# Performance work log

Measured on AMD Instinct MI355X. Metric: run time of the kernel, lower is better.

Reference implementation:

```python
import jax, jax.numpy as jnp
import numpy as np


def setup_inputs() -> dict:
    key = jax.random.key(0)
    ks = jax.random.split(key, 4)
    B, C, H, W = 8, 512, 128, 128
    K, D = 150, 512
    std = 0.02
    return {
        "x": jax.random.normal(ks[0], (B, C, H, W), dtype=jnp.float32),
        "cls_repr": jax.random.normal(ks[1], (1, K, D), dtype=jnp.float32) * std,
        "W_cls": jax.random.normal(ks[2], (D, D), dtype=jnp.float32) * std,
        "W_feat": jax.random.normal(ks[3], (D, D), dtype=jnp.float32) * std,
        "ln_gamma": jnp.ones((K,), dtype=jnp.float32),
        "ln_beta": jnp.zeros((K,), dtype=jnp.float32),
    }


def reference(x, cls_repr, W_cls, W_feat, ln_gamma, ln_beta):
    b, c, h, w = x.shape
    K = cls_repr.shape[1]
    # img_feat: [b, hw, c]
    img_feat = jnp.transpose(x, (0, 2, 3, 1)).reshape(b, h * w, c)
    cls = jnp.broadcast_to(cls_repr, (b, K, c))
    # coupled_attn: [b, K, hw]
    coupled_attn = jnp.einsum("bnc,bkc->bkn", img_feat, cls)
    # class-direction softmax over hw, feeds class offsets
    cls_attn = jax.nn.softmax(coupled_attn, axis=2)                 # [b,K,hw]
    cls_offset = jnp.einsum("bkn,bnc->bkc", cls_attn, img_feat) @ W_cls.T
    aligned_cls = cls + cls_offset                                   # [b,K,c]
    # position-direction softmax over K, feeds feature offsets
    pos_attn = jax.nn.softmax(coupled_attn, axis=1)                 # [b,K,hw]
    feat_offset = jnp.einsum("bkn,bkc->bnc", pos_attn, cls) @ W_feat.T
    aligned_feat = img_feat + feat_offset                            # [b,hw,c]
    # masks: [b, hw, K], LayerNorm over K
    masks = jnp.einsum("bnc,bkc->bnk", aligned_feat, aligned_cls)
    mu = jnp.mean(masks, axis=-1, keepdims=True)
    var = jnp.var(masks, axis=-1, keepdims=True)
    masks = (masks - mu) * jax.lax.rsqrt(var + 1e-5) * ln_gamma + ln_beta
    return jnp.transpose(masks, (0, 2, 1)).reshape(b, K, h, w)
```

## Files before the change

kernel.cpp:

```cpp
#include <hip/hip_runtime.h>
#include <math.h>

#define BB 8
#define CC 512
#define HWN 16384
#define KK 150
#define KP 160
#define NSEG 16
#define SEGN (HWN / NSEG)

typedef short bf8v __attribute__((ext_vector_type(8)));
typedef float f4v __attribute__((ext_vector_type(4)));

static __device__ inline unsigned short f2b(float f) {
  unsigned u = __float_as_uint(f);
  u += 0x7fffu + ((u >> 16) & 1u);
  return (unsigned short)(u >> 16);
}
static __device__ inline float b2f(unsigned short s) {
  return __uint_as_float(((unsigned)s) << 16);
}
static __device__ inline float b2fs(short s) { return b2f((unsigned short)s); }

__global__ __launch_bounds__(256) void t0_prep(const float* __restrict__ cls,
                                               const float* __restrict__ Wc,
                                               const float* __restrict__ Wf,
                                               unsigned short* __restrict__ cls16,
                                               unsigned short* __restrict__ Wc16,
                                               unsigned short* __restrict__ Wf16,
                                               unsigned short* __restrict__ MT16,
                                               unsigned short* __restrict__ AC16) {
  int i = blockIdx.x * 256 + threadIdx.x;
  if (i < KP * CC) {
    int k = i >> 9, c = i & 511;
    cls16[i] = (k < KK) ? f2b(cls[k * CC + c]) : 0;
  }
  if (i < BB * KP * KP) MT16[i] = 0;
  if (i < BB * (KP - KK) * CC) {
    int b = i / ((KP - KK) * CC);
    int r = i % ((KP - KK) * CC);
    int k = KK + (r >> 9);
    int c = r & 511;
    AC16[((size_t)b * KP + k) * CC + c] = 0;
  }
  if (i < CC * CC) {
    Wc16[i] = f2b(Wc[i]);
    Wf16[i] = f2b(Wf[i]);
  }
}

__global__ __launch_bounds__(256) void t1_transpose(const float* __restrict__ x,
                                                    unsigned short* __restrict__ xT,
                                                    unsigned short* __restrict__ x16) {
  __shared__ float ts[32][65];
  const int n0 = blockIdx.x * 64, c0 = blockIdx.y * 32, b = blockIdx.z;
  const int tid = threadIdx.x;
  const float* xb = x + (size_t)b * CC * HWN;
  unsigned short* x16o = x16 + (size_t)b * CC * HWN;
#pragma unroll
  for (int i = 0; i < 8; i++) {
    int e = tid + i * 256;
    int n = e & 63, c = e >> 6;
    float v = xb[(size_t)(c0 + c) * HWN + n0 + n];
    ts[c][n] = v;
    x16o[(size_t)(c0 + c) * HWN + n0 + n] = f2b(v);
  }
  __syncthreads();
  unsigned short* xo = xT + (size_t)b * HWN * CC;
#pragma unroll
  for (int i = 0; i < 4; i++) {
    int e = tid + i * 256;
    int c2 = e & 15, n = e >> 4;
    unsigned vv = (unsigned)f2b(ts[2 * c2][n]) | ((unsigned)f2b(ts[2 * c2 + 1][n]) << 16);
    *(unsigned*)&xo[(size_t)(n0 + n) * CC + c0 + 2 * c2] = vv;
  }
}

__global__ __launch_bounds__(256) void g1_mfma(const unsigned short* __restrict__ xT,
                                               const unsigned short* __restrict__ cls16,
                                               unsigned short* __restrict__ E16,
                                               unsigned short* __restrict__ ET16,
                                               float* __restrict__ vvec) {
  const int n0 = blockIdx.x * 128, b = blockIdx.y;
  const int tid = threadIdx.x, w = tid >> 6, L = tid & 63;
  const int q = L >> 4, m16 = L & 15;
  f4v zf = {0.f, 0.f, 0.f, 0.f};
  f4v acc[10][2];
#pragma unroll
  for (int mt = 0; mt < 10; mt++) { acc[mt][0] = zf; acc[mt][1] = zf; }
  const unsigned short* xr0 = xT + ((size_t)(b * HWN + n0 + 32 * w + m16)) * CC + 8 * q;
  const unsigned short* xr1 = xr0 + 16 * CC;
  const unsigned short* cb = cls16 + (size_t)m16 * CC + 8 * q;
#pragma unroll 2
  for (int c0 = 0; c0 < CC; c0 += 32) {
    bf8v b0 = *(const bf8v*)(xr0 + c0);
    bf8v b1 = *(const bf8v*)(xr1 + c0);
#pragma unroll
    for (int mt = 0; mt < 10; mt++) {
      bf8v a = *(const bf8v*)(cb + (size_t)(16 * mt) * CC + c0);
      acc[mt][0] = __builtin_amdgcn_mfma_f32_16x16x32_bf16(a, b0, acc[mt][0], 0, 0, 0);
      acc[mt][1] = __builtin_amdgcn_mfma_f32_16x16x32_bf16(a, b1, acc[mt][1], 0, 0, 0);
    }
  }
  float cs0 = 0.f, cs1 = 0.f;
#pragma unroll
  for (int mt = 0; mt < 10; mt++)
#pragma unroll
    for (int r = 0; r < 4; r++) {
      int k = 16 * mt + 4 * q + r;
      bool valid = k < KK;
      float e0 = valid ? __expf(acc[mt][0][r]) : 0.f;
      float e1 = valid ? __expf(acc[mt][1][r]) : 0.f;
      acc[mt][0][r] = e0;
      acc[mt][1][r] = e1;
      cs0 += e0;
      cs1 += e1;
    }
#pragma unroll
  for (int mt = 0; mt < 10; mt++)
#pragma unroll
    for (int r = 0; r < 4; r++) {
      int k = 16 * mt + 4 * q + r;
      size_t row = ((size_t)(b * KP + k)) * HWN + n0 + 32 * w;
      E16[row + m16] = f2b(acc[mt][0][r]);
      E16[row + 16 + m16] = f2b(acc[mt][1][r]);
    }
  const int nA = n0 + 32 * w + m16;
#pragma unroll
  for (int mt = 0; mt < 10; mt++) {
    unsigned lo0 = (unsigned)f2b(acc[mt][0][0]) | ((unsigned)f2b(acc[mt][0][1]) << 16);
    unsigned hi0 = (unsigned)f2b(acc[mt][0][2]) | ((unsigned)f2b(acc[mt][0][3]) << 16);
    unsigned lo1 = (unsigned)f2b(acc[mt][1][0]) | ((unsigned)f2b(acc[mt][1][1]) << 16);
    unsigned hi1 = (unsigned)f2b(acc[mt][1][2]) | ((unsigned)f2b(acc[mt][1][3]) << 16);
    size_t eoff = ((size_t)(b * HWN + nA)) * KP + 16 * mt + 4 * q;
    *(uint2*)&ET16[eoff] = make_uint2(lo0, hi0);
    *(uint2*)&ET16[eoff + (size_t)16 * KP] = make_uint2(lo1, hi1);
  }
  cs0 += __shfl_xor(cs0, 16, 64);
  cs0 += __shfl_xor(cs0, 32, 64);
  cs1 += __shfl_xor(cs1, 16, 64);
  cs1 += __shfl_xor(cs1, 32, 64);
  if (q == 0) {
    vvec[b * HWN + nA] = 1.0f / cs0;
    vvec[b * HWN + nA + 16] = 1.0f / cs1;
  }
}

__global__ __launch_bounds__(256) void g2_rowsum(const unsigned short* __restrict__ E16,
                                                 float* __restrict__ rowsum) {
  const int bk = blockIdx.x;
  const int b = bk / KK, k = bk % KK;
  const bf8v* row = (const bf8v*)(E16 + ((size_t)(b * KP + k)) * HWN);
  __shared__ float red[4];
  const int tid = threadIdx.x, lane = tid & 63, w = tid >> 6;
  float s = 0.f;
  for (int i = tid; i < HWN / 8; i += 256) {
    bf8v u = row[i];
#pragma unroll
    for (int j = 0; j < 8; j++) s += b2fs(u[j]);
  }
#pragma unroll
  for (int o = 32; o > 0; o >>= 1) s += __shfl_down(s, o, 64);
  if (lane == 0) red[w] = s;
  __syncthreads();
  if (tid == 0) rowsum[bk] = red[0] + red[1] + red[2] + red[3];
}

__global__ __launch_bounds__(256) void g3_mfma(const unsigned short* __restrict__ x16,
                                               const unsigned short* __restrict__ E16,
                                               float* __restrict__ Scp) {
  const int cblk = blockIdx.x, seg = blockIdx.y, b = blockIdx.z;
  const int tid = threadIdx.x, w = tid >> 6, L = tid & 63;
  const int q = L >> 4, m16 = L & 15;
  f4v zf = {0.f, 0.f, 0.f, 0.f};
  f4v acc[10][2];
#pragma unroll
  for (int mt = 0; mt < 10; mt++) { acc[mt][0] = zf; acc[mt][1] = zf; }
  const unsigned short* eb = E16 + ((size_t)(b * KP + m16)) * HWN + 8 * q;
  const unsigned short* xb = x16 + ((size_t)(b * CC + cblk * 128 + 32 * w + m16)) * HWN + 8 * q;
  const int ns0 = seg * SEGN;
#pragma unroll 2
  for (int nc0 = ns0; nc0 < ns0 + SEGN; nc0 += 32) {
    bf8v x0 = *(const bf8v*)(xb + nc0);
    bf8v x1 = *(const bf8v*)(xb + (size_t)16 * HWN + nc0);
#pragma unroll
    for (int mt = 0; mt < 10; mt++) {
      bf8v a = *(const bf8v*)(eb + (size_t)(16 * mt) * HWN + nc0);
      acc[mt][0] = __builtin_amdgcn_mfma_f32_16x16x32_bf16(a, x0, acc[mt][0], 0, 0, 0);
      acc[mt][1] = __builtin_amdgcn_mfma_f32_16x16x32_bf16(a, x1, acc[mt][1], 0, 0, 0);
    }
  }
#pragma unroll
  for (int mt = 0; mt < 10; mt++)
#pragma unroll
    for (int cc = 0; cc < 2; cc++)
#pragma unroll
      for (int r = 0; r < 4; r++) {
        int k = 16 * mt + 4 * q + r;
        if (k < KK) {
          int c = cblk * 128 + 32 * w + 16 * cc + m16;
          Scp[(((size_t)(b * NSEG + seg)) * KK + k) * CC + c] = acc[mt][cc][r];
        }
      }
}

__global__ __launch_bounds__(256) void g5_reduce(const float* __restrict__ Scp,
                                                 const float* __restrict__ rowsum,
                                                 unsigned short* __restrict__ Sc16) {
  const int bk = blockIdx.x;
  const int b = bk / KK, k = bk % KK;
  const float inv = 1.0f / rowsum[bk];
  for (int c = threadIdx.x; c < CC; c += 256) {
    float s = 0.f;
    for (int g = 0; g < NSEG; g++)
      s += Scp[(((size_t)(b * NSEG + g)) * KK + k) * CC + c];
    Sc16[((size_t)b * KP + k) * CC + c] = f2b(s * inv);
  }
}

__global__ __launch_bounds__(256) void g4b_cwf(const unsigned short* __restrict__ cls16,
                                               const unsigned short* __restrict__ Wf16,
                                               unsigned short* __restrict__ CWf16) {
  const int tid = threadIdx.x, w = tid >> 6, L = tid & 63;
  const int q = L >> 4, m16 = L & 15;
  const int j0 = blockIdx.x * 128 + 32 * w;
  f4v zf = {0.f, 0.f, 0.f, 0.f};
  f4v acc[10][2];
#pragma unroll
  for (int mt = 0; mt < 10; mt++) { acc[mt][0] = zf; acc[mt][1] = zf; }
  const unsigned short* ar = cls16 + (size_t)m16 * CC + 8 * q;
  const unsigned short* br = Wf16 + (size_t)(j0 + m16) * CC + 8 * q;
#pragma unroll 2
  for (int c0 = 0; c0 < CC; c0 += 32) {
    bf8v b0 = *(const bf8v*)(br + c0);
    bf8v b1 = *(const bf8v*)(br + (size_t)16 * CC + c0);
#pragma unroll
    for (int mt = 0; mt < 10; mt++) {
      bf8v a = *(const bf8v*)(ar + (size_t)(16 * mt) * CC + c0);
      acc[mt][0] = __builtin_amdgcn_mfma_f32_16x16x32_bf16(a, b0, acc[mt][0], 0, 0, 0);
      acc[mt][1] = __builtin_amdgcn_mfma_f32_16x16x32_bf16(a, b1, acc[mt][1], 0, 0, 0);
    }
  }
#pragma unroll
  for (int mt = 0; mt < 10; mt++)
#pragma unroll
    for (int nc = 0; nc < 2; nc++)
#pragma unroll
      for (int r = 0; r < 4; r++) {
        int k1 = 16 * mt + 4 * q + r;
        int j = j0 + 16 * nc + m16;
        CWf16[(size_t)k1 * CC + j] = f2b(acc[mt][nc][r]);
      }
}

__global__ __launch_bounds__(256) void g4a_ac(const unsigned short* __restrict__ Sc16,
                                              const unsigned short* __restrict__ Wc16,
                                              const float* __restrict__ cls,
                                              unsigned short* __restrict__ AC16) {
  const int b = blockIdx.y;
  const int tid = threadIdx.x, w = tid >> 6, L = tid & 63;
  const int q = L >> 4, m16 = L & 15;
  const int j0 = blockIdx.x * 128 + 32 * w;
  f4v zf = {0.f, 0.f, 0.f, 0.f};
  f4v acc[10][2];
#pragma unroll
  for (int mt = 0; mt < 10; mt++) { acc[mt][0] = zf; acc[mt][1] = zf; }
  const unsigned short* ar = Sc16 + ((size_t)b * KP + m16) * CC + 8 * q;
  const unsigned short* br = Wc16 + (size_t)(j0 + m16) * CC + 8 * q;
#pragma unroll 2
  for (int c0 = 0; c0 < CC; c0 += 32) {
    bf8v b0 = *(const bf8v*)(br + c0);
    bf8v b1 = *(const bf8v*)(br + (size_t)16 * CC + c0);
#pragma unroll
    for (int mt = 0; mt < 10; mt++) {
      bf8v a = *(const bf8v*)(ar + (size_t)(16 * mt) * CC + c0);
      acc[mt][0] = __builtin_amdgcn_mfma_f32_16x16x32_bf16(a, b0, acc[mt][0], 0, 0, 0);
      acc[mt][1] = __builtin_amdgcn_mfma_f32_16x16x32_bf16(a, b1, acc[mt][1], 0, 0, 0);
    }
  }
#pragma unroll
  for (int mt = 0; mt < 10; mt++)
#pragma unroll
    for (int nc = 0; nc < 2; nc++)
#pragma unroll
      for (int r = 0; r < 4; r++) {
        int k = 16 * mt + 4 * q + r;
        if (k < KK) {
          int j = j0 + 16 * nc + m16;
          AC16[((size_t)b * KP + k) * CC + j] = f2b(cls[k * CC + j] + acc[mt][nc][r]);
        }
      }
}

__global__ __launch_bounds__(256) void g4c_m(const unsigned short* __restrict__ AC16,
                                             const unsigned short* __restrict__ CWf16,
                                             unsigned short* __restrict__ MT16) {
  const int b = blockIdx.y;
  const int tid = threadIdx.x, w = tid >> 6, L = tid & 63;
  const int q = L >> 4, m16 = L & 15;
  const int k1t = blockIdx.x * 64 + 16 * w;
  f4v zf = {0.f, 0.f, 0.f, 0.f};
  f4v acc[10];
#pragma unroll
  for (int mt = 0; mt < 10; mt++) acc[mt] = zf;
  const unsigned short* ar = AC16 + ((size_t)b * KP + m16) * CC + 8 * q;
  const unsigned short* br = CWf16 + (size_t)(k1t + m16) * CC + 8 * q;
#pragma unroll 2
  for (int c0 = 0; c0 < CC; c0 += 32) {
    bf8v bb = *(const bf8v*)(br + c0);
#pragma unroll
    for (int mt = 0; mt < 10; mt++) {
      bf8v a = *(const bf8v*)(ar + (size_t)(16 * mt) * CC + c0);
      acc[mt] = __builtin_amdgcn_mfma_f32_16x16x32_bf16(a, bb, acc[mt], 0, 0, 0);
    }
  }
  const int k1 = k1t + m16;
#pragma unroll
  for (int mt = 0; mt < 10; mt++)
#pragma unroll
    for (int r = 0; r < 4; r++) {
      int k2 = 16 * mt + 4 * q + r;
      if (k1 < KK) MT16[((size_t)b * KP + k2) * KP + k1] = f2b(acc[mt][r]);
    }
}

__global__ __launch_bounds__(256) void g6_mfma(
    const unsigned short* __restrict__ xT, const unsigned short* __restrict__ ET,
    const float* __restrict__ vvec, const unsigned short* __restrict__ AC16,
    const unsigned short* __restrict__ MT16, const float* __restrict__ gamma,
    const float* __restrict__ beta, float* __restrict__ out) {
  const int n0 = blockIdx.x * 128, b = blockIdx.y;
  const int tid = threadIdx.x, w = tid >> 6, L = tid & 63;
  const int q = L >> 4, m16 = L & 15;
  f4v zf = {0.f, 0.f, 0.f, 0.f};
  f4v acc[10][2];
#pragma unroll
  for (int mt = 0; mt < 10; mt++) { acc[mt][0] = zf; acc[mt][1] = zf; }

  const unsigned short* et0 = ET + ((size_t)(b * HWN + n0 + 32 * w + m16)) * KP + 8 * q;
  const unsigned short* et1 = et0 + 16 * KP;
  const unsigned short* mb = MT16 + (size_t)b * KP * KP + (size_t)m16 * KP + 8 * q;
#pragma unroll
  for (int kc = 0; kc < KP; kc += 32) {
    bf8v b0 = *(const bf8v*)(et0 + kc);
    bf8v b1 = *(const bf8v*)(et1 + kc);
#pragma unroll
    for (int mt = 0; mt < 10; mt++) {
      bf8v a = *(const bf8v*)(mb + (size_t)(16 * mt) * KP + kc);
      acc[mt][0] = __builtin_amdgcn_mfma_f32_16x16x32_bf16(a, b0, acc[mt][0], 0, 0, 0);
      acc[mt][1] = __builtin_amdgcn_mfma_f32_16x16x32_bf16(a, b1, acc[mt][1], 0, 0, 0);
    }
  }
  const float v0 = vvec[b * HWN + n0 + 32 * w + m16];
  const float v1 = vvec[b * HWN + n0 + 32 * w + 16 + m16];
#pragma unroll
  for (int mt = 0; mt < 10; mt++)
#pragma unroll
    for (int r = 0; r < 4; r++) {
      acc[mt][0][r] *= v0;
      acc[mt][1][r] *= v1;
    }

  const unsigned short* xr0 = xT + ((size_t)(b * HWN + n0 + 32 * w + m16)) * CC + 8 * q;
  const unsigned short* xr1 = xr0 + 16 * CC;
  const unsigned short* ab = AC16 + (size_t)b * KP * CC + (size_t)m16 * CC + 8 * q;
#pragma unroll 2
  for (int c0 = 0; c0 < CC; c0 += 32) {
    bf8v b0 = *(const bf8v*)(xr0 + c0);
    bf8v b1 = *(const bf8v*)(xr1 + c0);
#pragma unroll
    for (int mt = 0; mt < 10; mt++) {
      bf8v a = *(const bf8v*)(ab + (size_t)(16 * mt) * CC + c0);
      acc[mt][0] = __builtin_amdgcn_mfma_f32_16x16x32_bf16(a, b0, acc[mt][0], 0, 0, 0);
      acc[mt][1] = __builtin_amdgcn_mfma_f32_16x16x32_bf16(a, b1, acc[mt][1], 0, 0, 0);
    }
  }

  float s1[2] = {0.f, 0.f}, s2[2] = {0.f, 0.f};
#pragma unroll
  for (int mt = 0; mt < 10; mt++)
#pragma unroll
    for (int r = 0; r < 4; r++)
#pragma unroll
      for (int nc = 0; nc < 2; nc++) {
        float a = acc[mt][nc][r];
        s1[nc] += a;
        s2[nc] += a * a;
      }
#pragma unroll
  for (int nc = 0; nc < 2; nc++) {
    s1[nc] += __shfl_xor(s1[nc], 16, 64);
    s1[nc] += __shfl_xor(s1[nc], 32, 64);
    s2[nc] += __shfl_xor(s2[nc], 16, 64);
    s2[nc] += __shfl_xor(s2[nc], 32, 64);
  }
  float mu[2], inv[2];
#pragma unroll
  for (int nc = 0; nc < 2; nc++) {
    mu[nc] = s1[nc] * (1.0f / KK);
    float var = s2[nc] * (1.0f / KK) - mu[nc] * mu[nc];
    inv[nc] = rsqrtf(var + 1e-5f);
  }
#pragma unroll
  for (int mt = 0; mt < 10; mt++)
#pragma unroll
    for (int r = 0; r < 4; r++) {
      int k = 16 * mt + 4 * q + r;
      if (k < KK) {
        float g = gamma[k], be = beta[k];
        size_t row = (size_t)(b * KK + k) * HWN + n0 + 32 * w;
        out[row + m16] = (acc[mt][0][r] - mu[0]) * inv[0] * g + be;
        out[row + 16 + m16] = (acc[mt][1][r] - mu[1]) * inv[1] * g + be;
      }
    }
}

extern "C" void kernel_launch(void* const* d_in, const int* in_sizes, int n_in,
                              void* d_out, int out_size, void* d_ws, size_t ws_size,
                              hipStream_t stream) {
  const float* x = (const float*)d_in[0];
  const float* cls = (const float*)d_in[1];
  const float* Wc = (const float*)d_in[2];
  const float* Wf = (const float*)d_in[3];
  const float* gam = (const float*)d_in[4];
  const float* bet = (const float*)d_in[5];
  float* out = (float*)d_out;

  char* p = (char*)d_ws;
  auto alloc = [&](size_t bytes) {
    char* r = p;
    p += (bytes + 255) & ~(size_t)255;
    return r;
  };
  unsigned short* xT16 = (unsigned short*)alloc((size_t)BB * HWN * CC * 2);
  unsigned short* x16 = (unsigned short*)alloc((size_t)BB * CC * HWN * 2);
  unsigned short* E16 = (unsigned short*)alloc((size_t)BB * KP * HWN * 2);
  unsigned short* ET16 = (unsigned short*)alloc((size_t)BB * HWN * KP * 2);
  float* Scp = (float*)alloc((size_t)BB * NSEG * KK * CC * 4);
  unsigned short* Sc16 = (unsigned short*)alloc((size_t)BB * KP * CC * 2);
  unsigned short* AC16 = (unsigned short*)alloc((size_t)BB * KP * CC * 2);
  unsigned short* CWf16 = (unsigned short*)alloc((size_t)192 * CC * 2);
  unsigned short* cls16 = (unsigned short*)alloc((size_t)KP * CC * 2);
  unsigned short* Wc16 = (unsigned short*)alloc((size_t)CC * CC * 2);
  unsigned short* Wf16 = (unsigned short*)alloc((size_t)CC * CC * 2);
  unsigned short* MT16 = (unsigned short*)alloc((size_t)BB * KP * KP * 2);
  float* rowsum = (float*)alloc(BB * KK * 4);
  float* vvec = (float*)alloc((size_t)BB * HWN * 4);

  t0_prep<<<dim3((CC * CC + 255) / 256), 256, 0, stream>>>(cls, Wc, Wf, cls16, Wc16,
                                                           Wf16, MT16, AC16);
  t1_transpose<<<dim3(HWN / 64, CC / 32, BB), 256, 0, stream>>>(x, xT16, x16);
  g1_mfma<<<dim3(HWN / 128, BB), 256, 0, stream>>>(xT16, cls16, E16, ET16, vvec);
  g2_rowsum<<<dim3(BB * KK), 256, 0, stream>>>(E16, rowsum);
  g4b_cwf<<<dim3(CC / 128), 256, 0, stream>>>(cls16, Wf16, CWf16);
  g3_mfma<<<dim3(CC / 128, NSEG, BB), 256, 0, stream>>>(x16, E16, Scp);
  g5_reduce<<<dim3(BB * KK), 256, 0, stream>>>(Scp, rowsum, Sc16);
  g4a_ac<<<dim3(CC / 128, BB), 256, 0, stream>>>(Sc16, Wc16, cls, AC16);
  g4c_m<<<dim3(3, BB), 256, 0, stream>>>(AC16, CWf16, MT16);
  g6_mfma<<<dim3(HWN / 128, BB), 256, 0, stream>>>(xT16, ET16, vvec, AC16, MT16,
                                                   gam, bet, out);
}
```

Measured before the change: 867.9 us.

## Widen MFMA n-tiles to 64 per wave and vectorize transpose loads

The g1 and g6 MFMA kernels now give each wave 64 spatial columns (four 16-wide tiles) instead of 32. Each A-fragment load from the class or matrix operand is therefore reused across four MFMAs, which cuts global/L2 traffic for that operand, and the grid halves. The transpose kernel switches to float4 loads and ushort4 stores to raise memory efficiency. The cost is doubled accumulator register use (160 floats), which lowers occupancy and could cause spills, and fewer blocks per batch.

```diff
diff --git a/kernel.cpp b/kernel.cpp
--- a/kernel.cpp
+++ b/kernel.cpp
@@ -58,21 +58,33 @@
   const float* xb = x + (size_t)b * CC * HWN;
   unsigned short* x16o = x16 + (size_t)b * CC * HWN;
 #pragma unroll
-  for (int i = 0; i < 8; i++) {
+  for (int i = 0; i < 2; i++) {
     int e = tid + i * 256;
-    int n = e & 63, c = e >> 6;
-    float v = xb[(size_t)(c0 + c) * HWN + n0 + n];
-    ts[c][n] = v;
-    x16o[(size_t)(c0 + c) * HWN + n0 + n] = f2b(v);
+    int c = e >> 4, n4 = (e & 15) * 4;
+    float4 v = *(const float4*)&xb[(size_t)(c0 + c) * HWN + n0 + n4];
+    ts[c][n4] = v.x;
+    ts[c][n4 + 1] = v.y;
+    ts[c][n4 + 2] = v.z;
+    ts[c][n4 + 3] = v.w;
+    ushort4 pk;
+    pk.x = f2b(v.x);
+    pk.y = f2b(v.y);
+    pk.z = f2b(v.z);
+    pk.w = f2b(v.w);
+    *(ushort4*)&x16o[(size_t)(c0 + c) * HWN + n0 + n4] = pk;
   }
   __syncthreads();
   unsigned short* xo = xT + (size_t)b * HWN * CC;
 #pragma unroll
-  for (int i = 0; i < 4; i++) {
+  for (int i = 0; i < 2; i++) {
     int e = tid + i * 256;
-    int c2 = e & 15, n = e >> 4;
-    unsigned vv = (unsigned)f2b(ts[2 * c2][n]) | ((unsigned)f2b(ts[2 * c2 + 1][n]) << 16);
-    *(unsigned*)&xo[(size_t)(n0 + n) * CC + c0 + 2 * c2] = vv;
+    int cg = e & 7, n = e >> 3;
+    ushort4 pk;
+    pk.x = f2b(ts[4 * cg][n]);
+    pk.y = f2b(ts[4 * cg + 1][n]);
+    pk.z = f2b(ts[4 * cg + 2][n]);
+    pk.w = f2b(ts[4 * cg + 3][n]);
+    *(ushort4*)&xo[(size_t)(n0 + n) * CC + c0 + 4 * cg] = pk;
   }
 }
 
@@ -81,68 +93,74 @@
                                                unsigned short* __restrict__ E16,
                                                unsigned short* __restrict__ ET16,
                                                float* __restrict__ vvec) {
-  const int n0 = blockIdx.x * 128, b = blockIdx.y;
-  const int tid = threadIdx.x, w = tid >> 6, L = tid & 63;
-  const int q = L >> 4, m16 = L & 15;
-  f4v zf = {0.f, 0.f, 0.f, 0.f};
-  f4v acc[10][2];
-#pragma unroll
-  for (int mt = 0; mt < 10; mt++) { acc[mt][0] = zf; acc[mt][1] = zf; }
-  const unsigned short* xr0 = xT + ((size_t)(b * HWN + n0 + 32 * w + m16)) * CC + 8 * q;
-  const unsigned short* xr1 = xr0 + 16 * CC;
+  const int n0 = blockIdx.x * 256, b = blockIdx.y;
+  const int tid = threadIdx.x, w = tid >> 6, L = tid & 63;
+  const int q = L >> 4, m16 = L & 15;
+  f4v zf = {0.f, 0.f, 0.f, 0.f};
+  f4v acc[10][4];
+#pragma unroll
+  for (int mt = 0; mt < 10; mt++)
+#pragma unroll
+    for (int nc = 0; nc < 4; nc++) acc[mt][nc] = zf;
+  const unsigned short* xr = xT + ((size_t)(b * HWN + n0 + 64 * w + m16)) * CC + 8 * q;
   const unsigned short* cb = cls16 + (size_t)m16 * CC + 8 * q;
 #pragma unroll 2
   for (int c0 = 0; c0 < CC; c0 += 32) {
-    bf8v b0 = *(const bf8v*)(xr0 + c0);
-    bf8v b1 = *(const bf8v*)(xr1 + c0);
+    bf8v bv[4];
+#pragma unroll
+    for (int nc = 0; nc < 4; nc++)
+      bv[nc] = *(const bf8v*)(xr + (size_t)(16 * nc) * CC + c0);
 #pragma unroll
     for (int mt = 0; mt < 10; mt++) {
       bf8v a = *(const bf8v*)(cb + (size_t)(16 * mt) * CC + c0);
-      acc[mt][0] = __builtin_amdgcn_mfma_f32_16x16x32_bf16(a, b0, acc[mt][0], 0, 0, 0);
-      acc[mt][1] = __builtin_amdgcn_mfma_f32_16x16x32_bf16(a, b1, acc[mt][1], 0, 0, 0);
-    }
-  }
-  float cs0 = 0.f, cs1 = 0.f;
+#pragma unroll
+      for (int nc = 0; nc < 4; nc++)
+        acc[mt][nc] = __builtin_amdgcn_mfma_f32_16x16x32_bf16(a, bv[nc], acc[mt][nc], 0, 0, 0);
+    }
+  }
+  float cs[4] = {0.f, 0.f, 0.f, 0.f};
 #pragma unroll
   for (int mt = 0; mt < 10; mt++)
 #pragma unroll
     for (int r = 0; r < 4; r++) {
       int k = 16 * mt + 4 * q + r;
       bool valid = k < KK;
-      float e0 = valid ? __expf(acc[mt][0][r]) : 0.f;
-      float e1 = valid ? __expf(acc[mt][1][r]) : 0.f;
-      acc[mt][0][r] = e0;
-      acc[mt][1][r] = e1;
-      cs0 += e0;
-      cs1 += e1;
+#pragma unroll
+      for (int nc = 0; nc < 4; nc++) {
+        float e = valid ? __expf(acc[mt][nc][r]) : 0.f;
+        acc[mt][nc][r] = e;
+        cs[nc] += e;
+      }
     }
 #pragma unroll
   for (int mt = 0; mt < 10; mt++)
 #pragma unroll
     for (int r = 0; r < 4; r++) {
       int k = 16 * mt + 4 * q + r;
-      size_t row = ((size_t)(b * KP + k)) * HWN + n0 + 32 * w;
-      E16[row + m16] = f2b(acc[mt][0][r]);
-      E16[row + 16 + m16] = f2b(acc[mt][1][r]);
-    }
-  const int nA = n0 + 32 * w + m16;
-#pragma unroll
-  for (int mt = 0; mt < 10; mt++) {
-    unsigned lo0 = (unsigned)f2b(acc[mt][0][0]) | ((unsigned)f2b(acc[mt][0][1]) << 16);
-    unsigned hi0 = (unsigned)f2b(acc[mt][0][2]) | ((unsigned)f2b(acc[mt][0][3]) << 16);
-    unsigned lo1 = (unsigned)f2b(acc[mt][1][0]) | ((unsigned)f2b(acc[mt][1][1]) << 16);
-    unsigned hi1 = (unsigned)f2b(acc[mt][1][2]) | ((unsigned)f2b(acc[mt][1][3]) << 16);
-    size_t eoff = ((size_t)(b * HWN + nA)) * KP + 16 * mt + 4 * q;
-    *(uint2*)&ET16[eoff] = make_uint2(lo0, hi0);
-    *(uint2*)&ET16[eoff + (size_t)16 * KP] = make_uint2(lo1, hi1);
-  }
-  cs0 += __shfl_xor(cs0, 16, 64);
-  cs0 += __shfl_xor(cs0, 32, 64);
-  cs1 += __shfl_xor(cs1, 16, 64);
-  cs1 += __shfl_xor(cs1, 32, 64);
+      size_t row = ((size_t)(b * KP + k)) * HWN + n0 + 64 * w;
+#pragma unroll
+      for (int nc = 0; nc < 4; nc++)
+        E16[row + 16 * nc + m16] = f2b(acc[mt][nc][r]);
+    }
+  const int nA = n0 + 64 * w + m16;
+#pragma unroll
+  for (int mt = 0; mt < 10; mt++)
+#pragma unroll
+    for (int nc = 0; nc < 4; nc++) {
+      unsigned lo = (unsigned)f2b(acc[mt][nc][0]) | ((unsigned)f2b(acc[mt][nc][1]) << 16);
+      unsigned hi = (unsigned)f2b(acc[mt][nc][2]) | ((unsigned)f2b(acc[mt][nc][3]) << 16);
+      size_t eoff = ((size_t)(b * HWN + nA + 16 * nc)) * KP + 16 * mt + 4 * q;
+      *(uint2*)&ET16[eoff] = make_uint2(lo, hi);
+    }
+#pragma unroll
+  for (int nc = 0; nc < 4; nc++) {
+    cs[nc] += __shfl_xor(cs[nc], 16, 64);
+    cs[nc] += __shfl_xor(cs[nc], 32, 64);
+  }
   if (q == 0) {
-    vvec[b * HWN + nA] = 1.0f / cs0;
-    vvec[b * HWN + nA + 16] = 1.0f / cs1;
+#pragma unroll
+    for (int nc = 0; nc < 4; nc++)
+      vvec[b * HWN + nA + 16 * nc] = 1.0f / cs[nc];
   }
 }
 
@@ -329,74 +347,80 @@
     const float* __restrict__ vvec, const unsigned short* __restrict__ AC16,
     const unsigned short* __restrict__ MT16, const float* __restrict__ gamma,
     const float* __restrict__ beta, float* __restrict__ out) {
-  const int n0 = blockIdx.x * 128, b = blockIdx.y;
-  const int tid = threadIdx.x, w = tid >> 6, L = tid & 63;
-  const int q = L >> 4, m16 = L & 15;
-  f4v zf = {0.f, 0.f, 0.f, 0.f};
-  f4v acc[10][2];
-#pragma unroll
-  for (int mt = 0; mt < 10; mt++) { acc[mt][0] = zf; acc[mt][1] = zf; }
-
-  const unsigned short* et0 = ET + ((size_t)(b * HWN + n0 + 32 * w + m16)) * KP + 8 * q;
-  const unsigned short* et1 = et0 + 16 * KP;
+  const int n0 = blockIdx.x * 256, b = blockIdx.y;
+  const int tid = threadIdx.x, w = tid >> 6, L = tid & 63;
+  const int q = L >> 4, m16 = L & 15;
+  f4v zf = {0.f, 0.f, 0.f, 0.f};
+  f4v acc[10][4];
+#pragma unroll
+  for (int mt = 0; mt < 10; mt++)
+#pragma unroll
+    for (int nc = 0; nc < 4; nc++) acc[mt][nc] = zf;
+
+  const unsigned short* et = ET + ((size_t)(b * HWN + n0 + 64 * w + m16)) * KP + 8 * q;
   const unsigned short* mb = MT16 + (size_t)b * KP * KP + (size_t)m16 * KP + 8 * q;
 #pragma unroll
   for (int kc = 0; kc < KP; kc += 32) {
-    bf8v b0 = *(const bf8v*)(et0 + kc);
-    bf8v b1 = *(const bf8v*)(et1 + kc);
+    bf8v bv[4];
+#pragma unroll
+    for (int nc = 0; nc < 4; nc++)
+      bv[nc] = *(const bf8v*)(et + (size_t)(16 * nc) * KP + kc);
 #pragma unroll
     for (int mt = 0; mt < 10; mt++) {
       bf8v a = *(const bf8v*)(mb + (size_t)(16 * mt) * KP + kc);
-      acc[mt][0] = __builtin_amdgcn_mfma_f32_16x16x32_bf16(a, b0, acc[mt][0], 0, 0, 0);
-      acc[mt][1] = __builtin_amdgcn_mfma_f32_16x16x32_bf16(a, b1, acc[mt][1], 0, 0, 0);
-    }
-  }
-  const float v0 = vvec[b * HWN + n0 + 32 * w + m16];
-  const float v1 = vvec[b * HWN + n0 + 32 * w + 16 + m16];
-#pragma unroll
-  for (int mt = 0; mt < 10; mt++)
-#pragma unroll
-    for (int r = 0; r < 4; r++) {
-      acc[mt][0][r] *= v0;
-      acc[mt][1][r] *= v1;
-    }
-
-  const unsigned short* xr0 = xT + ((size_t)(b * HWN + n0 + 32 * w + m16)) * CC + 8 * q;
-  const unsigned short* xr1 = xr0 + 16 * CC;
+#pragma unroll
+      for (int nc = 0; nc < 4; nc++)
+        acc[mt][nc] = __builtin_amdgcn_mfma_f32_16x16x32_bf16(a, bv[nc], acc[mt][nc], 0, 0, 0);
+    }
+  }
+  float vs[4];
+#pragma unroll
+  for (int nc = 0; nc < 4; nc++) vs[nc] = vvec[b * HWN + n0 + 64 * w + 16 * nc + m16];
+#pragma unroll
+  for (int mt = 0; mt < 10; mt++)
+#pragma unroll
+    for (int nc = 0; nc < 4; nc++)
+#pragma unroll
+      for (int r = 0; r < 4; r++) acc[mt][nc][r] *= vs[nc];
+
+  const unsigned short* xr = xT + ((size_t)(b * HWN + n0 + 64 * w + m16)) * CC + 8 * q;
   const unsigned short* ab = AC16 + (size_t)b * KP * CC + (size_t)m16 * CC + 8 * q;
 #pragma unroll 2
   for (int c0 = 0; c0 < CC; c0 += 32) {
-    bf8v b0 = *(const bf8v*)(xr0 + c0);
-    bf8v b1 = *(const bf8v*)(xr1 + c0);
+    bf8v bv[4];
+#pragma unroll
+    for (int nc = 0; nc < 4; nc++)
+      bv[nc] = *(const bf8v*)(xr + (size_t)(16 * nc) * CC + c0);
 #pragma unroll
     for (int mt = 0; mt < 10; mt++) {
       bf8v a = *(const bf8v*)(ab + (size_t)(16 * mt) * CC + c0);
-      acc[mt][0] = __builtin_amdgcn_mfma_f32_16x16x32_bf16(a, b0, acc[mt][0], 0, 0, 0);
-      acc[mt][1] = __builtin_amdgcn_mfma_f32_16x16x32_bf16(a, b1, acc[mt][1], 0, 0, 0);
-    }
-  }
-
-  float s1[2] = {0.f, 0.f}, s2[2] = {0.f, 0.f};
+#pragma unroll
+      for (int nc = 0; nc < 4; nc++)
+        acc[mt][nc] = __builtin_amdgcn_mfma_f32_16x16x32_bf16(a, bv[nc], acc[mt][nc], 0, 0, 0);
+    }
+  }
+
+  float s1[4] = {0.f, 0.f, 0.f, 0.f}, s2[4] = {0.f, 0.f, 0.f, 0.f};
 #pragma unroll
   for (int mt = 0; mt < 10; mt++)
 #pragma unroll
     for (int r = 0; r < 4; r++)
 #pragma unroll
-      for (int nc = 0; nc < 2; nc++) {
+      for (int nc = 0; nc < 4; nc++) {
         float a = acc[mt][nc][r];
         s1[nc] += a;
         s2[nc] += a * a;
       }
 #pragma unroll
-  for (int nc = 0; nc < 2; nc++) {
+  for (int nc = 0; nc < 4; nc++) {
     s1[nc] += __shfl_xor(s1[nc], 16, 64);
     s1[nc] += __shfl_xor(s1[nc], 32, 64);
     s2[nc] += __shfl_xor(s2[nc], 16, 64);
     s2[nc] += __shfl_xor(s2[nc], 32, 64);
   }
-  float mu[2], inv[2];
-#pragma unroll
-  for (int nc = 0; nc < 2; nc++) {
+  float mu[4], inv[4];
+#pragma unroll
+  for (int nc = 0; nc < 4; nc++) {
     mu[nc] = s1[nc] * (1.0f / KK);
     float var = s2[nc] * (1.0f / KK) - mu[nc] * mu[nc];
     inv[nc] = rsqrtf(var + 1e-5f);
@@ -408,9 +432,10 @@
       int k = 16 * mt + 4 * q + r;
       if (k < KK) {
         float g = gamma[k], be = beta[k];
-        size_t row = (size_t)(b * KK + k) * HWN + n0 + 32 * w;
-        out[row + m16] = (acc[mt][0][r] - mu[0]) * inv[0] * g + be;
-        out[row + 16 + m16] = (acc[mt][1][r] - mu[1]) * inv[1] * g + be;
+        size_t row = (size_t)(b * KK + k) * HWN + n0 + 64 * w;
+#pragma unroll
+        for (int nc = 0; nc < 4; nc++)
+          out[row + 16 * nc + m16] = (acc[mt][nc][r] - mu[nc]) * inv[nc] * g + be;
       }
     }
 }
@@ -450,13 +475,13 @@
   t0_prep<<<dim3((CC * CC + 255) / 256), 256, 0, stream>>>(cls, Wc, Wf, cls16, Wc16,
                                                            Wf16, MT16, AC16);
   t1_transpose<<<dim3(HWN / 64, CC / 32, BB), 256, 0, stream>>>(x, xT16, x16);
-  g1_mfma<<<dim3(HWN / 128, BB), 256, 0, stream>>>(xT16, cls16, E16, ET16, vvec);
+  g1_mfma<<<dim3(HWN / 256, BB), 256, 0, stream>>>(xT16, cls16, E16, ET16, vvec);
   g2_rowsum<<<dim3(BB * KK), 256, 0, stream>>>(E16, rowsum);
   g4b_cwf<<<dim3(CC / 128), 256, 0, stream>>>(cls16, Wf16, CWf16);
   g3_mfma<<<dim3(CC / 128, NSEG, BB), 256, 0, stream>>>(x16, E16, Scp);
   g5_reduce<<<dim3(BB * KK), 256, 0, stream>>>(Scp, rowsum, Sc16);
   g4a_ac<<<dim3(CC / 128, BB), 256, 0, stream>>>(Sc16, Wc16, cls, AC16);
   g4c_m<<<dim3(3, BB), 256, 0, stream>>>(AC16, CWf16, MT16);
-  g6_mfma<<<dim3(HWN / 128, BB), 256, 0, stream>>>(xT16, ET16, vvec, AC16, MT16,
+  g6_mfma<<<dim3(HWN / 256, BB), 256, 0, stream>>>(xT16, ET16, vvec, AC16, MT16,
                                                    gam, bet, out);
 }
```

Result: no change. 853.0 us (-1.7%).

## Double-buffer xT tiles into LDS via direct global-to-LDS loads; vectorize transpose

Applied to the files above, without the earlier changes.

The two xT-consuming GEMM kernels (g1 and g6) now stage 128x32 bf16 tiles of xT into a double-buffered, XOR-swizzled LDS buffer using global_load_lds. The load for the next step is issued while MFMAs run on the current one, and in g6 the first stage is prefetched during the earlier ET×MT GEMM. The transpose kernel switches to float4 reads and ushort4 writes to cut the number of memory instructions. The cost is extra LDS use and a block barrier on every K-step, which may reduce occupancy.

```diff
diff --git a/kernel.cpp b/kernel.cpp
--- a/kernel.cpp
+++ b/kernel.cpp
@@ -21,6 +21,12 @@
   return __uint_as_float(((unsigned)s) << 16);
 }
 static __device__ inline float b2fs(short s) { return b2f((unsigned short)s); }
+
+typedef const __attribute__((address_space(1))) void* gas_p;
+typedef __attribute__((address_space(3))) void* las_p;
+static __device__ __forceinline__ void gload16(const void* gp, void* lp) {
+  __builtin_amdgcn_global_load_lds((gas_p)gp, (las_p)lp, 16, 0, 0);
+}
 
 __global__ __launch_bounds__(256) void t0_prep(const float* __restrict__ cls,
                                                const float* __restrict__ Wc,
@@ -58,21 +64,33 @@
   const float* xb = x + (size_t)b * CC * HWN;
   unsigned short* x16o = x16 + (size_t)b * CC * HWN;
 #pragma unroll
-  for (int i = 0; i < 8; i++) {
+  for (int i = 0; i < 2; i++) {
     int e = tid + i * 256;
-    int n = e & 63, c = e >> 6;
-    float v = xb[(size_t)(c0 + c) * HWN + n0 + n];
-    ts[c][n] = v;
-    x16o[(size_t)(c0 + c) * HWN + n0 + n] = f2b(v);
+    int c = e >> 4, n4 = (e & 15) * 4;
+    float4 v = *(const float4*)&xb[(size_t)(c0 + c) * HWN + n0 + n4];
+    ts[c][n4] = v.x;
+    ts[c][n4 + 1] = v.y;
+    ts[c][n4 + 2] = v.z;
+    ts[c][n4 + 3] = v.w;
+    ushort4 pk;
+    pk.x = f2b(v.x);
+    pk.y = f2b(v.y);
+    pk.z = f2b(v.z);
+    pk.w = f2b(v.w);
+    *(ushort4*)&x16o[(size_t)(c0 + c) * HWN + n0 + n4] = pk;
   }
   __syncthreads();
   unsigned short* xo = xT + (size_t)b * HWN * CC;
 #pragma unroll
-  for (int i = 0; i < 4; i++) {
+  for (int i = 0; i < 2; i++) {
     int e = tid + i * 256;
-    int c2 = e & 15, n = e >> 4;
-    unsigned vv = (unsigned)f2b(ts[2 * c2][n]) | ((unsigned)f2b(ts[2 * c2 + 1][n]) << 16);
-    *(unsigned*)&xo[(size_t)(n0 + n) * CC + c0 + 2 * c2] = vv;
+    int cg = e & 7, n = e >> 3;
+    ushort4 pk;
+    pk.x = f2b(ts[4 * cg][n]);
+    pk.y = f2b(ts[4 * cg + 1][n]);
+    pk.z = f2b(ts[4 * cg + 2][n]);
+    pk.w = f2b(ts[4 * cg + 3][n]);
+    *(ushort4*)&xo[(size_t)(n0 + n) * CC + c0 + 4 * cg] = pk;
   }
 }
 
@@ -81,6 +99,7 @@
                                                unsigned short* __restrict__ E16,
                                                unsigned short* __restrict__ ET16,
                                                float* __restrict__ vvec) {
+  __shared__ unsigned short sB[2][128 * 32];
   const int n0 = blockIdx.x * 128, b = blockIdx.y;
   const int tid = threadIdx.x, w = tid >> 6, L = tid & 63;
   const int q = L >> 4, m16 = L & 15;
@@ -88,19 +107,43 @@
   f4v acc[10][2];
 #pragma unroll
   for (int mt = 0; mt < 10; mt++) { acc[mt][0] = zf; acc[mt][1] = zf; }
-  const unsigned short* xr0 = xT + ((size_t)(b * HWN + n0 + 32 * w + m16)) * CC + 8 * q;
-  const unsigned short* xr1 = xr0 + 16 * CC;
   const unsigned short* cb = cls16 + (size_t)m16 * CC + 8 * q;
-#pragma unroll 2
-  for (int c0 = 0; c0 < CC; c0 += 32) {
-    bf8v b0 = *(const bf8v*)(xr0 + c0);
-    bf8v b1 = *(const bf8v*)(xr1 + c0);
-#pragma unroll
-    for (int mt = 0; mt < 10; mt++) {
-      bf8v a = *(const bf8v*)(cb + (size_t)(16 * mt) * CC + c0);
-      acc[mt][0] = __builtin_amdgcn_mfma_f32_16x16x32_bf16(a, b0, acc[mt][0], 0, 0, 0);
-      acc[mt][1] = __builtin_amdgcn_mfma_f32_16x16x32_bf16(a, b1, acc[mt][1], 0, 0, 0);
-    }
+  const int sr0 = w * 32 + (L >> 2);
+  const int sch = L & 3;
+  const unsigned short* xbase = xT + (size_t)(b * HWN + n0) * CC;
+
+#define G1_STAGE(buf, c0)                                                      \
+  {                                                                            \
+    _Pragma("unroll") for (int j = 0; j < 2; j++) {                            \
+      int row = sr0 + j * 16;                                                  \
+      int ch = sch ^ ((row >> 1) & 3);                                         \
+      gload16(xbase + (size_t)row * CC + (c0) + ch * 8,                        \
+              &sB[buf][(w * 32 + j * 16) * 32]);                               \
+    }                                                                          \
+  }
+
+  G1_STAGE(0, 0);
+  __syncthreads();
+  for (int s = 0; s < 16; s++) {
+    if (s < 15) G1_STAGE((s + 1) & 1, (s + 1) * 32);
+    const int cur = s & 1;
+    bf8v a[10];
+#pragma unroll
+    for (int mt = 0; mt < 10; mt++)
+      a[mt] = *(const bf8v*)(cb + (size_t)(16 * mt) * CC + s * 32);
+    bf8v bv[2];
+#pragma unroll
+    for (int cc = 0; cc < 2; cc++) {
+      int row = w * 32 + cc * 16 + m16;
+      int slot = q ^ ((row >> 1) & 3);
+      bv[cc] = *(const bf8v*)&sB[cur][row * 32 + slot * 8];
+    }
+#pragma unroll
+    for (int mt = 0; mt < 10; mt++) {
+      acc[mt][0] = __builtin_amdgcn_mfma_f32_16x16x32_bf16(a[mt], bv[0], acc[mt][0], 0, 0, 0);
+      acc[mt][1] = __builtin_amdgcn_mfma_f32_16x16x32_bf16(a[mt], bv[1], acc[mt][1], 0, 0, 0);
+    }
+    __syncthreads();
   }
   float cs0 = 0.f, cs1 = 0.f;
 #pragma unroll
@@ -329,6 +372,7 @@
     const float* __restrict__ vvec, const unsigned short* __restrict__ AC16,
     const unsigned short* __restrict__ MT16, const float* __restrict__ gamma,
     const float* __restrict__ beta, float* __restrict__ out) {
+  __shared__ unsigned short sB[2][128 * 32];
   const int n0 = blockIdx.x * 128, b = blockIdx.y;
   const int tid = threadIdx.x, w = tid >> 6, L = tid & 63;
   const int q = L >> 4, m16 = L & 15;
@@ -337,6 +381,20 @@
 #pragma unroll
   for (int mt = 0; mt < 10; mt++) { acc[mt][0] = zf; acc[mt][1] = zf; }
 
+  const int sr0 = w * 32 + (L >> 2);
+  const int sch = L & 3;
+  const unsigned short* xbase = xT + (size_t)(b * HWN + n0) * CC;
+#define G6_STAGE(buf, c0)                                                      \
+  {                                                                            \
+    _Pragma("unroll") for (int j = 0; j < 2; j++) {                            \
+      int row = sr0 + j * 16;                                                  \
+      int ch = sch ^ ((row >> 1) & 3);                                         \
+      gload16(xbase + (size_t)row * CC + (c0) + ch * 8,                        \
+              &sB[buf][(w * 32 + j * 16) * 32]);                               \
+    }                                                                          \
+  }
+  G6_STAGE(0, 0);
+
   const unsigned short* et0 = ET + ((size_t)(b * HWN + n0 + 32 * w + m16)) * KP + 8 * q;
   const unsigned short* et1 = et0 + 16 * KP;
   const unsigned short* mb = MT16 + (size_t)b * KP * KP + (size_t)m16 * KP + 8 * q;
@@ -361,19 +419,28 @@
       acc[mt][1][r] *= v1;
     }
 
-  const unsigned short* xr0 = xT + ((size_t)(b * HWN + n0 + 32 * w + m16)) * CC + 8 * q;
-  const unsigned short* xr1 = xr0 + 16 * CC;
   const unsigned short* ab = AC16 + (size_t)b * KP * CC + (size_t)m16 * CC + 8 * q;
-#pragma unroll 2
-  for (int c0 = 0; c0 < CC; c0 += 32) {
-    bf8v b0 = *(const bf8v*)(xr0 + c0);
-    bf8v b1 = *(const bf8v*)(xr1 + c0);
-#pragma unroll
-    for (int mt = 0; mt < 10; mt++) {
-      bf8v a = *(const bf8v*)(ab + (size_t)(16 * mt) * CC + c0);
-      acc[mt][0] = __builtin_amdgcn_mfma_f32_16x16x32_bf16(a, b0, acc[mt][0], 0, 0, 0);
-      acc[mt][1] = __builtin_amdgcn_mfma_f32_16x16x32_bf16(a, b1, acc[mt][1], 0, 0, 0);
-    }
+  __syncthreads();
+  for (int s = 0; s < 16; s++) {
+    if (s < 15) G6_STAGE((s + 1) & 1, (s + 1) * 32);
+    const int cur = s & 1;
+    bf8v a[10];
+#pragma unroll
+    for (int mt = 0; mt < 10; mt++)
+      a[mt] = *(const bf8v*)(ab + (size_t)(16 * mt) * CC + s * 32);
+    bf8v bv[2];
+#pragma unroll
+    for (int cc = 0; cc < 2; cc++) {
+      int row = w * 32 + cc * 16 + m16;
+      int slot = q ^ ((row >> 1) & 3);
+      bv[cc] = *(const bf8v*)&sB[cur][row * 32 + slot * 8];
+    }
+#pragma unroll
+    for (int mt = 0; mt < 10; mt++) {
+      acc[mt][0] = __builtin_amdgcn_mfma_f32_16x16x32_bf16(a[mt], bv[0], acc[mt][0], 0, 0, 0);
+      acc[mt][1] = __builtin_amdgcn_mfma_f32_16x16x32_bf16(a[mt], bv[1], acc[mt][1], 0, 0, 0);
+    }
+    __syncthreads();
   }
 
   float s1[2] = {0.f, 0.f}, s2[2] = {0.f, 0.f};
```

Result: slower. 945.1 us (+8.9%).
